# Optimization experiments

Hardware: AMD Instinct MI355X
Metric: run time of the kernel (lower is better)

The kernel has to match this reference:

```python
import math
import jax, jax.numpy as jnp
import numpy as np

B, C, F_, W = 4, 2, 512, 1024
NH = 8
HD = F_ // NH            # 64 head dim
ROT = HD // 2            # 32 rotated dims
NFREQ = ROT // 2         # 16 base freqs ('pixel': linspace(1, max_freq/2, dim//2)*pi)


def mc_linear(x, w_pw):
    # x: [b,c,f_in,w], w_pw: [c, f_out, f_in] -> [b,c,f_out,w]
    return jnp.einsum('bchw,cgh->bcgw', x, w_pw)


def apply_rope(t, freqs):
    # t: [b,c,n,w,d]; freqs: [w, rot_dim] (already pair-repeated)
    rot_dim = freqs.shape[-1]
    t_rot, t_pass = t[..., :rot_dim], t[..., rot_dim:]
    cos, sin = jnp.cos(freqs), jnp.sin(freqs)
    x1, x2 = t_rot[..., 0::2], t_rot[..., 1::2]
    rh = jnp.stack([-x2, x1], axis=-1).reshape(t_rot.shape)  # rotate_half (interleaved pairs)
    return jnp.concatenate([t_rot * cos + rh * sin, t_pass], axis=-1)


def setup_inputs() -> dict:
    key = jax.random.key(0)
    ks = jax.random.split(key, 6)
    x = jax.random.normal(ks[0], (B, C, F_, W), dtype=jnp.float32)
    bound = 1.0 / math.sqrt(F_)
    def w(k):
        return jax.random.uniform(k, (C, F_, F_), minval=-bound, maxval=bound, dtype=jnp.float32)
    wq, wk, wv, wo = w(ks[1]), w(ks[2]), w(ks[3]), w(ks[4])
    # learned 'pixel' freqs: linspace(1., max_freq/2=5., NFREQ) * pi
    freqs_param = (jnp.linspace(1.0, 5.0, NFREQ) * math.pi).astype(jnp.float32)
    return {"x": x, "wq": wq, "wk": wk, "wv": wv, "wo": wo, "freqs_param": freqs_param}


def reference(x, wq, wk, wv, wo, freqs_param):
    b, c, h, w = x.shape
    def heads(t):  # [b,c,h,w] -> [b,c,NH,w,HD]
        return t.transpose(0, 1, 3, 2).reshape(b, c, w, NH, HD).transpose(0, 1, 3, 2, 4)
    pos = jnp.arange(w, dtype=jnp.float32)
    freqs = jnp.repeat(pos[:, None] * freqs_param[None, :], 2, axis=-1)  # [w, ROT]
    # NOTE: original module uses q_proj for q, k, and v (k_proj/v_proj unused)
    q = apply_rope(heads(mc_linear(x, wq)), freqs)
    k = apply_rope(heads(mc_linear(x, wq)), freqs)
    v = heads(mc_linear(x, wq))
    qk = jnp.einsum('bcnqd,bcnkd->bcnqk', q, k) / math.sqrt(h)
    a = jnp.einsum('bcnqk,bcnkd->bcnqd', jax.nn.softmax(qk, axis=-1), v)
    a = a.transpose(0, 1, 3, 2, 4).reshape(b, c, w, NH * HD).transpose(0, 1, 3, 2)  # [b,c,h,w]
    return mc_linear(a, wo)
```

## Files before the change

### kernel.cpp

```cpp
#include <hip/hip_runtime.h>
#include <hip/hip_bf16.h>
#include <math.h>

#define B_ 4
#define C_ 2
#define F_ 512
#define W_ 1024
#define NH_ 8
#define HD_ 64
#define ROT_ 32
#define NFREQ_ 16
#define BC_ (B_*C_)

#define QSC_ 0.2525048f

typedef short bf16x8 __attribute__((ext_vector_type(8)));
typedef float f32x4  __attribute__((ext_vector_type(4)));
typedef float f32x16 __attribute__((ext_vector_type(16)));
typedef unsigned short u16;
typedef unsigned int   u32;

#if __has_builtin(__builtin_amdgcn_exp2f)
#define EXP2(x) __builtin_amdgcn_exp2f(x)
#else
#define EXP2(x) exp2f(x)
#endif

#define VDRAIN() asm volatile("s_waitcnt vmcnt(0)" ::: "memory")

__device__ __forceinline__ u16 f2bf(float f) {
    union { float f; u32 u; } v; v.f = f;
    u32 r = (v.u + 0x7fffu + ((v.u >> 16) & 1u)) >> 16;
    return (u16)r;
}
__device__ __forceinline__ float bf2f(u16 h) {
    union { u32 u; float f; } v; v.u = ((u32)h) << 16;
    return v.f;
}
__device__ __forceinline__ f32x4 mfma16(bf16x8 a, bf16x8 b, f32x4 c) {
    return __builtin_amdgcn_mfma_f32_16x16x32_bf16(a, b, c, 0, 0, 0);
}
__device__ __forceinline__ f32x16 mfma32(bf16x8 a, bf16x8 b, f32x16 c) {
    return __builtin_amdgcn_mfma_f32_32x32x16_bf16(a, b, c, 0, 0, 0);
}
__device__ __forceinline__ void gload16(const u16* g, u16* l) {
    __builtin_amdgcn_global_load_lds(
        (const __attribute__((address_space(1))) u32*)g,
        (__attribute__((address_space(3))) u32*)l, 16, 0, 0);
}
__device__ __forceinline__ u32 pk2(float lo, float hi) {
    __hip_bfloat162 h = __float22bfloat162_rn(make_float2(lo, hi));
    union { __hip_bfloat162 b; u32 u; } cv; cv.b = h; return cv.u;
}
__device__ __forceinline__ void pl32swap(u32& a, u32& b) {
    asm volatile("v_permlane32_swap_b32 %0, %1" : "+v"(a), "+v"(b));
}

__global__ __launch_bounds__(256)
void prep_all(const float* __restrict__ wq, const float* __restrict__ wo,
              const float* __restrict__ fp, const float* __restrict__ x,
              u16* __restrict__ wqh, u16* __restrict__ woh, u16* __restrict__ wol,
              float2* __restrict__ trig, u16* __restrict__ xh)
{
    __shared__ float T[64][65];
    const int b = blockIdx.x, t = threadIdx.x;
    if (b < 512) {
        int i = (b * 256 + t) * 4;
        float4 v = *(const float4*)(wq + i);
        ushort4 h;
        h.x = f2bf(v.x); h.y = f2bf(v.y); h.z = f2bf(v.z); h.w = f2bf(v.w);
        *(ushort4*)(wqh + i) = h;
    } else if (b < 1024) {
        int i = ((b - 512) * 256 + t) * 4;
        float4 v = *(const float4*)(wo + i);
        ushort4 h, l;
        h.x = f2bf(v.x); l.x = f2bf(v.x - bf2f(h.x));
        h.y = f2bf(v.y); l.y = f2bf(v.y - bf2f(h.y));
        h.z = f2bf(v.z); l.z = f2bf(v.z - bf2f(h.z));
        h.w = f2bf(v.w); l.w = f2bf(v.w - bf2f(h.w));
        *(ushort4*)(woh + i) = h;
        *(ushort4*)(wol + i) = l;
    } else if (b < 1088) {
        int idx = (b - 1024) * 256 + t;
        int w = idx >> 4, j = idx & 15;
        float th = (float)w * fp[j];
        float s, c;
        sincosf(th, &s, &c);
        trig[idx] = make_float2(c, s);
    } else {
        const int b2 = b - 1088;
        const int h0 = (b2 & 7) * 64, w0 = ((b2 >> 3) & 15) * 64, bc = b2 >> 7;
        {
            const int hl = t >> 2, wc = (t & 3) * 16;
            const float* src = x + ((size_t)bc * F_ + h0 + hl) * W_ + w0 + wc;
            #pragma unroll
            for (int z = 0; z < 4; ++z)
                *(float4*)(&T[hl][wc + z * 4]) = *(const float4*)(src + z * 4);
        }
        __syncthreads();
        {
            const int wl = t >> 2, hc = (t & 3) * 16;
            u16 hv[16];
            #pragma unroll
            for (int z = 0; z < 16; ++z) hv[z] = f2bf(T[hc + z][wl]);
            size_t base = ((size_t)bc * W_ + w0 + wl) * F_ + h0 + hc;
            *(uint4*)(xh + base)     = *(uint4*)(hv);
            *(uint4*)(xh + base + 8) = *(uint4*)(hv + 8);
        }
    }
}

template<int MODE>
__global__ __launch_bounds__(256)
void gemm4(const u16* __restrict__ Ah_, const u16* __restrict__ Al_,
           const u16* __restrict__ Bh_, const u16* __restrict__ Bl_,
           u16* __restrict__ Vout, u16* __restrict__ Qout,
           float* __restrict__ Fout, const float2* __restrict__ trig)
{
    constexpr int BUFS = MODE ? 12288 : 6144;
    __shared__ u16 sh[2 * BUFS];

    const int tid = threadIdx.x, lane = tid & 63, wid = tid >> 6;
    const int wm = wid >> 1, wn = wid & 1;
    const int m0 = blockIdx.x * 64, n0 = blockIdx.y * 128, bc = blockIdx.z, c = bc % C_;
    const u16* Abh = Ah_ + (size_t)c * F_ * F_;
    const u16* Abl = MODE ? (Al_ + (size_t)c * F_ * F_) : (const u16*)nullptr;
    const u16* Bbh = Bh_ + (size_t)bc * W_ * F_;
    const u16* Bbl = MODE ? (Bl_ + (size_t)bc * W_ * F_) : (const u16*)nullptr;

    f32x4 acc[2][4] = {};
    const int srow = tid >> 2, sslot = tid & 3;

    auto STAGE = [&](int k0, int buf) {
        u16* base = sh + buf * BUFS;
        {
            const int ts = sslot ^ ((srow >> 1) & 3);
            const size_t ga = (size_t)(m0 + srow) * F_ + k0 + ts * 8;
            gload16(Abh + ga, base + wid * 512);
            if constexpr (MODE) gload16(Abl + ga, base + 6144 + wid * 512);
        }
        #pragma unroll
        for (int h = 0; h < 2; ++h) {
            const int brow = h * 64 + srow;
            const int ts = sslot ^ ((brow >> 1) & 3);
            const size_t gb = (size_t)(n0 + brow) * F_ + k0 + ts * 8;
            gload16(Bbh + gb, base + 2048 + h * 2048 + wid * 512);
            if constexpr (MODE) gload16(Bbl + gb, base + 8192 + h * 2048 + wid * 512);
        }
    };

    STAGE(0, 0);
    VDRAIN();
    __syncthreads();
    int cur = 0;
    for (int kt = 0; kt < 16; ++kt) {
        if (kt < 15) STAGE((kt + 1) * 32, cur ^ 1);
        const u16* Ash = sh + cur * BUFS;
        const u16* Bsh = Ash + 2048;
        const u16* Asl = Ash + 6144;
        const u16* Bsl = Ash + 8192;

        bf16x8 fah[2], fal[2];
        #pragma unroll
        for (int i = 0; i < 2; ++i) {
            const int row = wm * 32 + i * 16 + (lane & 15);
            const int idx = row * 32 + (((lane >> 4) ^ ((row >> 1) & 3)) << 3);
            fah[i] = *(const bf16x8*)(&Ash[idx]);
            if constexpr (MODE) fal[i] = *(const bf16x8*)(&Asl[idx]);
        }
        #pragma unroll
        for (int j = 0; j < 4; ++j) {
            const int rowb = wn * 64 + j * 16 + (lane & 15);
            const int idxb = rowb * 32 + (((lane >> 4) ^ ((rowb >> 1) & 3)) << 3);
            bf16x8 bh = *(const bf16x8*)(&Bsh[idxb]);
            #pragma unroll
            for (int i = 0; i < 2; ++i)
                acc[i][j] = mfma16(fah[i], bh, acc[i][j]);
            if constexpr (MODE) {
                bf16x8 bl = *(const bf16x8*)(&Bsl[idxb]);
                #pragma unroll
                for (int i = 0; i < 2; ++i) {
                    acc[i][j] = mfma16(fah[i], bl, acc[i][j]);
                    acc[i][j] = mfma16(fal[i], bh, acc[i][j]);
                }
            }
        }
        VDRAIN();
        __syncthreads();
        cur ^= 1;
    }

    #pragma unroll
    for (int i = 0; i < 2; ++i) {
        const int gr = m0 + wm * 32 + i * 16 + (lane >> 4) * 4;
        #pragma unroll
        for (int j = 0; j < 4; ++j) {
            const int wc = n0 + wn * 64 + j * 16 + (lane & 15);
            #pragma unroll
            for (int r = 0; r < 4; ++r) {
                const size_t ad = ((size_t)bc * F_ + gr + r) * W_ + wc;
                if constexpr (MODE == 1) Fout[ad] = acc[i][j][r];
                else                     Vout[ad] = f2bf(acc[i][j][r]);
            }
        }
    }

    if constexpr (MODE == 0) {
        __syncthreads();
        u16* Qt = sh + wid * 2048;
        const int head = blockIdx.x;
        #pragma unroll
        for (int j = 0; j < 4; ++j) {
            const int wl = j * 16 + (lane & 15);
            const int wg = n0 + wn * 64 + wl;
            #pragma unroll
            for (int i = 0; i < 2; ++i) {
                float q[4];
                if (wm == 0) {
                    #pragma unroll
                    for (int p = 0; p < 2; ++p) {
                        const int fidx = i * 8 + (lane >> 4) * 2 + p;
                        float2 cs = trig[wg * NFREQ_ + fidx];
                        float e = acc[i][j][2 * p], o = acc[i][j][2 * p + 1];
                        q[2 * p]     = (e * cs.x - o * cs.y) * QSC_;
                        q[2 * p + 1] = (o * cs.x + e * cs.y) * QSC_;
                    }
                } else {
                    #pragma unroll
                    for (int r = 0; r < 4; ++r) q[r] = acc[i][j][r] * QSC_;
                }
                #pragma unroll
                for (int r = 0; r < 4; ++r) {
                    const int ddl = i * 16 + (lane >> 4) * 4 + r;
                    Qt[wl * 32 + ((ddl & 7) | (((ddl >> 3) ^ (wl & 3)) << 3))] = f2bf(q[r]);
                }
            }
        }
        const size_t qrow = (((size_t)bc * NH_ + head) * W_ + n0 + wn * 64 + lane) * 64 + wm * 32;
        #pragma unroll
        for (int s = 0; s < 4; ++s) {
            uint4 v = *(const uint4*)(&Qt[lane * 32 + ((s ^ (lane & 3)) << 3)]);
            *(uint4*)(&Qout[qrow + s * 8]) = v;
        }
    }
}

__global__ __launch_bounds__(256)
void attn3(const u16* __restrict__ Qt, const u16* __restrict__ Vg,
           u16* __restrict__ Ah, u16* __restrict__ Al)
{
    __shared__ u16 sh[16384];
    const int tid = threadIdx.x, lane = tid & 63, wid = tid >> 6;
    const int q0 = blockIdx.x * 128, head = blockIdx.y, bc = blockIdx.z;
    const u16* qb = Qt + ((size_t)bc * NH_ + head) * W_ * 64;
    const u16* vb = Vg + ((size_t)bc * F_ + head * HD_) * W_;

    const int qcol = lane & 31, hi = lane >> 5;
    const int srow = lane >> 3, st = lane & 7;

    bf16x8 qf[4];
    {
        const u16* qrow = qb + (size_t)(q0 + wid * 32 + qcol) * 64 + hi * 8;
        #pragma unroll
        for (int ks = 0; ks < 4; ++ks)
            qf[ks] = *(const bf16x8*)(qrow + ks * 16);
    }

    f32x16 o0, o1;
    #pragma unroll
    for (int i = 0; i < 16; ++i) { o0[i] = 0.f; o1[i] = 0.f; }
    float lsum = 0.f;

    auto STAGE = [&](int kt, int buf) {
        const int k0 = kt * 64;
        u16* Ksb = sh + buf * 8192;
        u16* Vsb = Ksb + 4096;
        #pragma unroll
        for (int p = 0; p < 2; ++p) {
            const int rb = wid * 16 + p * 8;
            const int r  = rb + srow;
            const int ts = st ^ (r & 7);
            gload16(qb + (size_t)(k0 + r) * 64 + ts * 8, Ksb + rb * 64);
            gload16(vb + (size_t)r * W_ + k0 + ts * 8,   Vsb + rb * 64);
        }
    };

    STAGE(0, 0);
    VDRAIN();
    __syncthreads();
    int cur = 0;
    for (int kt = 0; kt < 16; ++kt) {
        if (kt < 15) STAGE(kt + 1, cur ^ 1);
        const u16* Ks = sh + cur * 8192;
        const u16* Vs = Ks + 4096;

        f32x16 s0, s1;
        #pragma unroll
        for (int i = 0; i < 16; ++i) { s0[i] = 0.f; s1[i] = 0.f; }
        #pragma unroll
        for (int ks = 0; ks < 4; ++ks) {
            const int sl = ks * 2 + hi;
            const int kA = qcol;
            const int kB = 32 + qcol;
            bf16x8 kf0 = *(const bf16x8*)(Ks + kA * 64 + ((sl ^ (kA & 7)) << 3));
            bf16x8 kf1 = *(const bf16x8*)(Ks + kB * 64 + ((sl ^ (kB & 7)) << 3));
            s0 = mfma32(kf0, qf[ks], s0);
            s1 = mfma32(kf1, qf[ks], s1);
        }

        float p0[16], p1[16];
        #pragma unroll
        for (int i = 0; i < 16; ++i) { p0[i] = EXP2(s0[i]); p1[i] = EXP2(s1[i]); }
        float part = 0.f;
        #pragma unroll
        for (int i = 0; i < 16; ++i) part += p0[i] + p1[i];
        lsum += part;

        bf16x8 pf[4];
        #pragma unroll
        for (int kb = 0; kb < 2; ++kb) {
            const float* pp = kb ? p1 : p0;
            #pragma unroll
            for (int f = 0; f < 2; ++f) {
                u32 a1 = pk2(pp[f*8+0], pp[f*8+1]);
                u32 a2 = pk2(pp[f*8+2], pp[f*8+3]);
                u32 b1 = pk2(pp[f*8+4], pp[f*8+5]);
                u32 b2 = pk2(pp[f*8+6], pp[f*8+7]);
                pl32swap(a1, b1);
                pl32swap(a2, b2);
                union { u32 w[4]; bf16x8 v; } u;
                u.w[0] = a1; u.w[1] = a2; u.w[2] = b1; u.w[3] = b2;
                pf[kb * 2 + f] = u.v;
            }
        }

        #pragma unroll
        for (int ks2 = 0; ks2 < 4; ++ks2) {
            const int sl = ks2 * 2 + hi;
            const int d0r = qcol;
            const int d1r = 32 + qcol;
            bf16x8 vf0 = *(const bf16x8*)(Vs + d0r * 64 + ((sl ^ (d0r & 7)) << 3));
            bf16x8 vf1 = *(const bf16x8*)(Vs + d1r * 64 + ((sl ^ (d1r & 7)) << 3));
            o0 = mfma32(vf0, pf[ks2], o0);
            o1 = mfma32(vf1, pf[ks2], o1);
        }
        VDRAIN();
        __syncthreads();
        cur ^= 1;
    }

    lsum += __shfl_xor(lsum, 32);
    const float inv = 1.f / lsum;

    const int wrow = q0 + wid * 32 + qcol;
    const size_t rowbase = ((size_t)bc * W_ + wrow) * F_ + head * HD_;
    #pragma unroll
    for (int dblk = 0; dblk < 2; ++dblk) {
        const f32x16 ov = dblk ? o1 : o0;
        const int coloff = dblk * 32;
        #pragma unroll
        for (int pr = 0; pr < 8; ++pr) {
            const float v1 = ov[2 * pr]     * inv;
            const float v2 = ov[2 * pr + 1] * inv;
            const int drow = ((2 * pr) & 3) + 8 * (pr >> 1) + 4 * hi;
            const u16 h1 = f2bf(v1), h2 = f2bf(v2);
            const u16 l1 = f2bf(v1 - bf2f(h1)), l2 = f2bf(v2 - bf2f(h2));
            *(u32*)(Ah + rowbase + coloff + drow) = (u32)h1 | ((u32)h2 << 16);
            *(u32*)(Al + rowbase + coloff + drow) = (u32)l1 | ((u32)l2 << 16);
        }
    }
}

extern "C" void kernel_launch(void* const* d_in, const int* in_sizes, int n_in,
                              void* d_out, int out_size, void* d_ws, size_t ws_size,
                              hipStream_t stream) {
    const float* x  = (const float*)d_in[0];
    const float* wq = (const float*)d_in[1];
    const float* wo = (const float*)d_in[4];
    const float* fp = (const float*)d_in[5];
    float* out = (float*)d_out;

    char* w8 = (char*)d_ws;
    const size_t MB = 1024 * 1024;
    u16* xh   = (u16*)(w8);
    u16* wqh  = (u16*)(w8 + 8 * MB);
    u16* woh  = (u16*)(w8 + 9 * MB);
    u16* wol  = (u16*)(w8 + 10 * MB);
    float2* trig = (float2*)(w8 + 11 * MB);
    u16* qbuf = (u16*)(w8 + 12 * MB);
    u16* vbuf = (u16*)(w8 + 20 * MB);
    u16* al   = (u16*)(w8 + 28 * MB);
    u16* ah   = xh;

    prep_all<<<2112, 256, 0, stream>>>(wq, wo, fp, x, wqh, woh, wol, trig, xh);

    gemm4<0><<<dim3(8, 8, 8), 256, 0, stream>>>(
        wqh, nullptr, xh, nullptr, vbuf, qbuf, nullptr, trig);

    attn3<<<dim3(W_ / 128, NH_, BC_), 256, 0, stream>>>(qbuf, vbuf, ah, al);

    gemm4<1><<<dim3(8, 8, 8), 256, 0, stream>>>(
        woh, wol, ah, al, nullptr, nullptr, out, nullptr);
}
```

Measured before the change: 150.8 us.

## Drop low-bf16 attention output split and read K fragments straight from global

The attention kernel no longer writes a low-order bf16 residual of its output. The output projection GEMM therefore drops the B-low operand, using two MFMA passes instead of three and less shared memory. The attention kernel is also reshaped to 128-thread blocks of 64 queries, staging only V in LDS while K fragments are loaded directly from global/L2 each iteration. This cuts memory traffic and MFMA work, at the cost of precision in the final projection and possibly less efficient, uncoalesced K loads.

```diff
diff --git a/kernel.cpp b/kernel.cpp
--- a/kernel.cpp
+++ b/kernel.cpp
@@ -113,11 +113,12 @@
 template<int MODE>
 __global__ __launch_bounds__(256)
 void gemm4(const u16* __restrict__ Ah_, const u16* __restrict__ Al_,
-           const u16* __restrict__ Bh_, const u16* __restrict__ Bl_,
+           const u16* __restrict__ Bh_,
            u16* __restrict__ Vout, u16* __restrict__ Qout,
            float* __restrict__ Fout, const float2* __restrict__ trig)
 {
-    constexpr int BUFS = MODE ? 12288 : 6144;
+    constexpr int BUFS  = MODE ? 8192 : 6144;
+    constexpr int B_OFF = MODE ? 4096 : 2048;
     __shared__ u16 sh[2 * BUFS];
 
     const int tid = threadIdx.x, lane = tid & 63, wid = tid >> 6;
@@ -126,7 +127,6 @@
     const u16* Abh = Ah_ + (size_t)c * F_ * F_;
     const u16* Abl = MODE ? (Al_ + (size_t)c * F_ * F_) : (const u16*)nullptr;
     const u16* Bbh = Bh_ + (size_t)bc * W_ * F_;
-    const u16* Bbl = MODE ? (Bl_ + (size_t)bc * W_ * F_) : (const u16*)nullptr;
 
     f32x4 acc[2][4] = {};
     const int srow = tid >> 2, sslot = tid & 3;
@@ -137,15 +137,14 @@
             const int ts = sslot ^ ((srow >> 1) & 3);
             const size_t ga = (size_t)(m0 + srow) * F_ + k0 + ts * 8;
             gload16(Abh + ga, base + wid * 512);
-            if constexpr (MODE) gload16(Abl + ga, base + 6144 + wid * 512);
+            if constexpr (MODE) gload16(Abl + ga, base + 2048 + wid * 512);
         }
         #pragma unroll
         for (int h = 0; h < 2; ++h) {
             const int brow = h * 64 + srow;
             const int ts = sslot ^ ((brow >> 1) & 3);
             const size_t gb = (size_t)(n0 + brow) * F_ + k0 + ts * 8;
-            gload16(Bbh + gb, base + 2048 + h * 2048 + wid * 512);
-            if constexpr (MODE) gload16(Bbl + gb, base + 8192 + h * 2048 + wid * 512);
+            gload16(Bbh + gb, base + B_OFF + h * 2048 + wid * 512);
         }
     };
 
@@ -156,9 +155,8 @@
     for (int kt = 0; kt < 16; ++kt) {
         if (kt < 15) STAGE((kt + 1) * 32, cur ^ 1);
         const u16* Ash = sh + cur * BUFS;
-        const u16* Bsh = Ash + 2048;
-        const u16* Asl = Ash + 6144;
-        const u16* Bsl = Ash + 8192;
+        const u16* Asl = Ash + 2048;
+        const u16* Bsh = Ash + B_OFF;
 
         bf16x8 fah[2], fal[2];
         #pragma unroll
@@ -177,12 +175,9 @@
             for (int i = 0; i < 2; ++i)
                 acc[i][j] = mfma16(fah[i], bh, acc[i][j]);
             if constexpr (MODE) {
-                bf16x8 bl = *(const bf16x8*)(&Bsl[idxb]);
                 #pragma unroll
-                for (int i = 0; i < 2; ++i) {
-                    acc[i][j] = mfma16(fah[i], bl, acc[i][j]);
+                for (int i = 0; i < 2; ++i)
                     acc[i][j] = mfma16(fal[i], bh, acc[i][j]);
-                }
             }
         }
         VDRAIN();
@@ -245,13 +240,13 @@
     }
 }
 
-__global__ __launch_bounds__(256)
-void attn3(const u16* __restrict__ Qt, const u16* __restrict__ Vg,
-           u16* __restrict__ Ah, u16* __restrict__ Al)
+__global__ __launch_bounds__(128)
+void attn4(const u16* __restrict__ Qt, const u16* __restrict__ Vg,
+           u16* __restrict__ AhO)
 {
-    __shared__ u16 sh[16384];
+    __shared__ u16 sh[8192];
     const int tid = threadIdx.x, lane = tid & 63, wid = tid >> 6;
-    const int q0 = blockIdx.x * 128, head = blockIdx.y, bc = blockIdx.z;
+    const int q0 = blockIdx.x * 64, head = blockIdx.y, bc = blockIdx.z;
     const u16* qb = Qt + ((size_t)bc * NH_ + head) * W_ * 64;
     const u16* vb = Vg + ((size_t)bc * F_ + head * HD_) * W_;
 
@@ -273,15 +268,13 @@
 
     auto STAGE = [&](int kt, int buf) {
         const int k0 = kt * 64;
-        u16* Ksb = sh + buf * 8192;
-        u16* Vsb = Ksb + 4096;
-        #pragma unroll
-        for (int p = 0; p < 2; ++p) {
-            const int rb = wid * 16 + p * 8;
+        u16* Vsb = sh + buf * 4096;
+        #pragma unroll
+        for (int p = 0; p < 4; ++p) {
+            const int rb = wid * 32 + p * 8;
             const int r  = rb + srow;
             const int ts = st ^ (r & 7);
-            gload16(qb + (size_t)(k0 + r) * 64 + ts * 8, Ksb + rb * 64);
-            gload16(vb + (size_t)r * W_ + k0 + ts * 8,   Vsb + rb * 64);
+            gload16(vb + (size_t)r * W_ + k0 + ts * 8, Vsb + rb * 64);
         }
     };
 
@@ -291,8 +284,8 @@
     int cur = 0;
     for (int kt = 0; kt < 16; ++kt) {
         if (kt < 15) STAGE(kt + 1, cur ^ 1);
-        const u16* Ks = sh + cur * 8192;
-        const u16* Vs = Ks + 4096;
+        const u16* Vs = sh + cur * 4096;
+        const int k0 = kt * 64;
 
         f32x16 s0, s1;
         #pragma unroll
@@ -300,10 +293,8 @@
         #pragma unroll
         for (int ks = 0; ks < 4; ++ks) {
             const int sl = ks * 2 + hi;
-            const int kA = qcol;
-            const int kB = 32 + qcol;
-            bf16x8 kf0 = *(const bf16x8*)(Ks + kA * 64 + ((sl ^ (kA & 7)) << 3));
-            bf16x8 kf1 = *(const bf16x8*)(Ks + kB * 64 + ((sl ^ (kB & 7)) << 3));
+            bf16x8 kf0 = *(const bf16x8*)(qb + (size_t)(k0 + qcol) * 64 + sl * 8);
+            bf16x8 kf1 = *(const bf16x8*)(qb + (size_t)(k0 + 32 + qcol) * 64 + sl * 8);
             s0 = mfma32(kf0, qf[ks], s0);
             s1 = mfma32(kf1, qf[ks], s1);
         }
@@ -364,9 +355,7 @@
             const float v2 = ov[2 * pr + 1] * inv;
             const int drow = ((2 * pr) & 3) + 8 * (pr >> 1) + 4 * hi;
             const u16 h1 = f2bf(v1), h2 = f2bf(v2);
-            const u16 l1 = f2bf(v1 - bf2f(h1)), l2 = f2bf(v2 - bf2f(h2));
-            *(u32*)(Ah + rowbase + coloff + drow) = (u32)h1 | ((u32)h2 << 16);
-            *(u32*)(Al + rowbase + coloff + drow) = (u32)l1 | ((u32)l2 << 16);
+            *(u32*)(AhO + rowbase + coloff + drow) = (u32)h1 | ((u32)h2 << 16);
         }
     }
 }
@@ -389,16 +378,15 @@
     float2* trig = (float2*)(w8 + 11 * MB);
     u16* qbuf = (u16*)(w8 + 12 * MB);
     u16* vbuf = (u16*)(w8 + 20 * MB);
-    u16* al   = (u16*)(w8 + 28 * MB);
     u16* ah   = xh;
 
     prep_all<<<2112, 256, 0, stream>>>(wq, wo, fp, x, wqh, woh, wol, trig, xh);
 
     gemm4<0><<<dim3(8, 8, 8), 256, 0, stream>>>(
-        wqh, nullptr, xh, nullptr, vbuf, qbuf, nullptr, trig);
-
-    attn3<<<dim3(W_ / 128, NH_, BC_), 256, 0, stream>>>(qbuf, vbuf, ah, al);
+        wqh, nullptr, xh, vbuf, qbuf, nullptr, trig);
+
+    attn4<<<dim3(16, NH_, BC_), 128, 0, stream>>>(qbuf, vbuf, ah);
 
     gemm4<1><<<dim3(8, 8, 8), 256, 0, stream>>>(
-        woh, wol, ah, al, nullptr, nullptr, out, nullptr);
-}
+        woh, wol, ah, nullptr, nullptr, out, trig);
+}
```

Measured after the change: 163.4 us. 8.4% more time.
